# Optimization experiments

Measured on AMD Instinct MI355X. Metric: run time of the kernel, lower is better.

The kernel has to match this reference:

```python
import jax, jax.numpy as jnp
import numpy as np

N_Q = 4       # n_qubits
PATCH = 3
PAD = 1       # patch_size // 2


def _u3(theta, phi, lam):
    # U3 gate matrix (2x2 complex)
    c = jnp.cos(theta / 2)
    s = jnp.sin(theta / 2)
    row0 = jnp.stack([c + 0j, -jnp.exp(1j * lam) * s])
    row1 = jnp.stack([jnp.exp(1j * phi) * s, jnp.exp(1j * (phi + lam)) * c])
    return jnp.stack([row0, row1]).astype(jnp.complex64)


def _apply_1q(state, U, wire):
    # state: (N,2,2,2,2) complex; U: (2,2) shared or (N,2,2) batched
    s = jnp.moveaxis(state, 1 + wire, -1)
    shp = s.shape
    s = s.reshape(s.shape[0], -1, 2)
    if U.ndim == 2:
        out = jnp.einsum('ij,nrj->nri', U, s)
    else:
        out = jnp.einsum('nij,nrj->nri', U, s)
    return jnp.moveaxis(out.reshape(shp), -1, 1 + wire)


def _apply_2q(state, U4, cw, tw):
    # U4: (4,4) on (control, target) subspace ordered |c t>
    s = jnp.moveaxis(state, (1 + cw, 1 + tw), (-2, -1))
    shp = s.shape
    s = s.reshape(s.shape[0], -1, 4)
    out = jnp.einsum('ij,nrj->nri', U4, s)
    return jnp.moveaxis(out.reshape(shp), (-2, -1), (1 + cw, 1 + tw))


def setup_inputs() -> dict:
    key = jax.random.key(0)
    ks = jax.random.split(key, 8)
    B, C, H, W = 16, 64, 64, 64
    out_ch = 128
    d_in = C * PATCH * PATCH  # 576
    x = jax.random.normal(ks[0], (B, C, H, W), dtype=jnp.float32)
    fc1_w = jax.random.normal(ks[1], (N_Q, d_in), dtype=jnp.float32) * (1.0 / np.sqrt(d_in))
    fc1_b = jax.random.normal(ks[2], (N_Q,), dtype=jnp.float32) * 0.01
    u3_params = jax.random.normal(ks[3], (N_Q, 3), dtype=jnp.float32)
    cu3_params = jax.random.normal(ks[4], (N_Q, 3), dtype=jnp.float32)
    fc_w = jax.random.normal(ks[5], (out_ch, N_Q), dtype=jnp.float32) * 0.5
    fc_b = jax.random.normal(ks[6], (out_ch,), dtype=jnp.float32) * 0.01
    return {"x": x, "fc1_w": fc1_w, "fc1_b": fc1_b, "u3_params": u3_params,
            "cu3_params": cu3_params, "fc_w": fc_w, "fc_b": fc_b}


def reference(x, fc1_w, fc1_b, u3_params, cu3_params, fc_w, fc_b):
    B, C, H, W = x.shape
    xp = jnp.pad(x, ((0, 0), (0, 0), (PAD, PAD), (PAD, PAD)))
    Hout, Wout = H, W  # stride 1, same padding
    # im2col: feature order (C, di, dj) matches torch patch.reshape(B,-1)
    cols = jnp.stack([xp[:, :, di:di + Hout, dj:dj + Wout]
                      for di in range(PATCH) for dj in range(PATCH)], axis=2)  # (B,C,9,H,W)
    patches = cols.transpose(0, 3, 4, 1, 2).reshape(B, Hout * Wout, C * PATCH * PATCH)
    ang = patches @ fc1_w.T + fc1_b  # (B, P, 4) rotation angles
    Np = B * Hout * Wout
    ang = ang.reshape(Np, N_Q)
    # initial state |0000> for every (batch, patch)
    state = jnp.zeros((Np, 2 ** N_Q), jnp.complex64).at[:, 0].set(1.0)
    state = state.reshape((Np,) + (2,) * N_Q)
    # RY encoding (per-element angles)
    for w in range(N_Q):
        th = ang[:, w] / 2
        c, s = jnp.cos(th), jnp.sin(th)
        Ury = jnp.stack([jnp.stack([c, -s], -1), jnp.stack([s, c], -1)], -2).astype(jnp.complex64)
        state = _apply_1q(state, Ury, w)
    # trainable U3 on every wire
    for w in range(N_Q):
        state = _apply_1q(state, _u3(u3_params[w, 0], u3_params[w, 1], u3_params[w, 2]), w)
    # circular CU3 ring (0,1),(1,2),(2,3),(3,0)
    for w in range(N_Q):
        U = _u3(cu3_params[w, 0], cu3_params[w, 1], cu3_params[w, 2])
        U4 = jnp.eye(4, dtype=jnp.complex64).at[2:, 2:].set(U)
        state = _apply_2q(state, U4, w, (w + 1) % N_Q)
    # <Z> on each wire
    probs = state.real ** 2 + state.imag ** 2  # (Np,2,2,2,2)
    zv = jnp.array([1.0, -1.0], jnp.float32)
    expz = jnp.stack(
        [(probs * zv.reshape((1,) + (1,) * w + (2,) + (1,) * (N_Q - 1 - w))).sum(axis=(1, 2, 3, 4))
         for w in range(N_Q)], axis=1)  # (Np,4)
    out = expz.reshape(B, Hout * Wout, N_Q) @ fc_w.T + fc_b  # (B,P,out_ch)
    out_ch = fc_w.shape[0]
    # faithful to original: view(B, out_ch, side_h, side_w) on contiguous (P,out_ch)
    return out.reshape(B, out_ch, Hout, Wout)
```

## Files before the change

kernel.cpp:

```cpp
#include <hip/hip_runtime.h>
#include <hip/hip_bf16.h>
#include <math.h>

typedef unsigned short u16;
typedef unsigned int   u32;
typedef unsigned long long u64;

__device__ inline float bfbits2f(u32 lo16) {
    u32 u = lo16 << 16;
    return __builtin_bit_cast(float, u);
}
__device__ inline float bchi(u32 w) {
    return __builtin_bit_cast(float, w & 0xffff0000u);
}
__device__ inline float bclo(u32 w) {
    return __builtin_bit_cast(float, w << 16);
}
__device__ inline u16 f2bf(float f) {
    u32 u = __builtin_bit_cast(u32, f);
    u = u + 0x7fffu + ((u >> 16) & 1u);
    return (u16)(u >> 16);
}
__device__ inline float ld_param(const void* p, int i, int isbf16) {
    return isbf16 ? bfbits2f(((const u16*)p)[i]) : ((const float*)p)[i];
}

__device__ inline int sniff_bf16(const void* x, int t) {
    u32 xv = ((const u32*)x)[t & 63];
    u32 e  = (xv >> 7) & 0xFFu;
    u64 m  = __ballot(e >= 110u && e <= 130u);
    return (__popcll(m) >= 32) ? 1 : 0;
}

__global__ __launch_bounds__(256) void kA_conv(
        const void* __restrict__ x, const void* __restrict__ fc1_w,
        void* __restrict__ out) {
    __shared__ u32 tile[24 * 34];
    __shared__ float4 red4[256];
    const int t = threadIdx.x;
    const int bid = blockIdx.x;
    const int cg  = bid & 7;
    const int row = (bid >> 3) & 63;
    const int b   = bid >> 9;
    const int rowblk = bid >> 3;
    const int c0 = cg * 8;
    const int tc = t >> 6;

    const int bf = sniff_bf16(x, t);

    const int cs = __builtin_amdgcn_readfirstlane(c0 + tc * 2);
    u32 w36[36];
    if (bf) {
        const u32* fw = (const u32*)fc1_w;
#pragma unroll
        for (int k = 0; k < 36; ++k) {
            int c = cs + (k >= 18 ? 1 : 0);
            int rem = k % 18; int r = rem / 6; int p = rem % 6;
            int i0 = 2 * p, i1 = i0 + 1;
            int q0 = i0 / 3, d0 = i0 - 3 * q0;
            int q1 = i1 / 3, d1 = i1 - 3 * q1;
            int a0 = q0 * 576 + c * 9 + r * 3 + d0;
            int a1 = q1 * 576 + c * 9 + r * 3 + d1;
            u32 lo = (fw[a0 >> 1] >> (16 * (a0 & 1))) & 0xffffu;
            u32 hi = (fw[a1 >> 1] >> (16 * (a1 & 1))) & 0xffffu;
            w36[k] = lo | (hi << 16);
        }
    } else {
        const float* ff = (const float*)fc1_w;
#pragma unroll
        for (int k = 0; k < 36; ++k) {
            int c = cs + (k >= 18 ? 1 : 0);
            int rem = k % 18; int r = rem / 6; int p = rem % 6;
            int i0 = 2 * p, i1 = i0 + 1;
            int q0 = i0 / 3, d0 = i0 - 3 * q0;
            int q1 = i1 / 3, d1 = i1 - 3 * q1;
            u32 lo = f2bf(ff[q0 * 576 + c * 9 + r * 3 + d0]);
            u32 hi = f2bf(ff[q1 * 576 + c * 9 + r * 3 + d1]);
            w36[k] = lo | (hi << 16);
        }
    }

    const u32*    xu = (const u32*)x;
    const float2* xf = (const float2*)x;
    const int xbase = b * 131072;

    {
        const int jj = t & 31;
        const int g8 = t >> 5;
#pragma unroll
        for (int i = 0; i < 3; ++i) {
            int rowcl = g8 + i * 8;
            int r = rowcl >> 3, cl = rowcl & 7;
            int gr = row - 1 + r;
            u32 pk = 0;
            if (gr >= 0 && gr < 64) {
                int idx = xbase + (c0 + cl) * 2048 + gr * 32 + jj;
                if (bf) pk = xu[idx];
                else { float2 v = xf[idx];
                       pk = (u32)f2bf(v.x) | ((u32)f2bf(v.y) << 16); }
            }
            tile[rowcl * 34 + 1 + jj] = pk;
        }
        if (t < 48) { int rc = t >> 1; tile[rc * 34 + ((t & 1) ? 33 : 0)] = 0u; }
    }
    __syncthreads();

    const int j = t & 63;
    const int pj = (j + 1) >> 1;
    const int sh = (1 - (j & 1)) * 16;
    float ang0 = 0.f, ang1 = 0.f, ang2 = 0.f, ang3 = 0.f;
#pragma unroll
    for (int cc = 0; cc < 2; ++cc) {
        const int cl = tc * 2 + cc;
#pragma unroll
        for (int r = 0; r < 3; ++r) {
            const u32* rp = tile + (r * 8 + cl) * 34 + pj;
            u32 lo = rp[0], hi = rp[1];
            u64 v = (((u64)hi << 32) | lo) >> sh;
            u32 vlo = (u32)v, vhi = (u32)(v >> 32);
            float e0 = bclo(vlo);
            float e1 = bchi(vlo);
            float e2 = bclo(vhi);
            const int wb = cc * 18 + r * 6;
            u32 u0 = w36[wb], u1 = w36[wb + 1], u2 = w36[wb + 2];
            u32 u3 = w36[wb + 3], u4 = w36[wb + 4], u5 = w36[wb + 5];
            ang0 += e0 * bclo(u0) + e1 * bchi(u0) + e2 * bclo(u1);
            ang1 += e0 * bchi(u1) + e1 * bclo(u2) + e2 * bchi(u2);
            ang2 += e0 * bclo(u3) + e1 * bchi(u3) + e2 * bclo(u4);
            ang3 += e0 * bchi(u4) + e1 * bclo(u5) + e2 * bchi(u5);
        }
    }

    red4[tc * 64 + j] = make_float4(ang0, ang1, ang2, ang3);
    __syncthreads();
    if (t < 64) {
        float4 a0 = red4[t], a1 = red4[64 + t], a2 = red4[128 + t], a3 = red4[192 + t];
        float4 s = make_float4(a0.x + a1.x + a2.x + a3.x,
                               a0.y + a1.y + a2.y + a3.y,
                               a0.z + a1.z + a2.z + a3.z,
                               a0.w + a1.w + a2.w + a3.w);
        float4* part = (float4*)out;
        const int C = bf ? 1024 : 2048;
        part[rowblk * C + cg * 64 + t] = s;
    }
}

__global__ __launch_bounds__(256) void kB_circuit_fc(
        const void* __restrict__ x,
        const void* __restrict__ fc1_b, const void* __restrict__ u3p,
        const void* __restrict__ cu3p,  const void* __restrict__ fc_w,
        const void* __restrict__ fc_b,  void* __restrict__ out) {
    __shared__ float smG[64];
    __shared__ float4 smEz[64];
    const int t = threadIdx.x;
    const int bf = sniff_bf16(x, t);
    const int C = bf ? 1024 : 2048;
    const int base = blockIdx.x * C;

    float angf[4] = {0.f, 0.f, 0.f, 0.f};
    if (t < 64) {
        const float4* part = (const float4*)out;
        float ax = 0.f, ay = 0.f, az = 0.f, aw = 0.f;
#pragma unroll
        for (int g = 0; g < 8; ++g) {
            float4 a = part[base + g * 64 + t];
            ax += a.x; ay += a.y; az += a.z; aw += a.w;
        }
        angf[0] = ld_param(fc1_b, 0, bf) + ax;
        angf[1] = ld_param(fc1_b, 1, bf) + ay;
        angf[2] = ld_param(fc1_b, 2, bf) + az;
        angf[3] = ld_param(fc1_b, 3, bf) + aw;
    }
    if (t < 8) {
        int w = t & 3;
        const void* p = (t < 4) ? u3p : cu3p;
        float th = ld_param(p, w * 3 + 0, bf);
        float ph = ld_param(p, w * 3 + 1, bf);
        float la = ld_param(p, w * 3 + 2, bf);
        float c = cosf(0.5f * th), s = sinf(0.5f * th);
        float cl = cosf(la), sl = sinf(la);
        float cp = cosf(ph), sp = sinf(ph);
        float cpl = cp * cl - sp * sl, spl = sp * cl + cp * sl;
        float* m = smG + t * 8;
        m[0] = c;        m[1] = 0.f;
        m[2] = -cl * s;  m[3] = -sl * s;
        m[4] = cp * s;   m[5] = sp * s;
        m[6] = cpl * c;  m[7] = spl * c;
    }
    __syncthreads();

    if (t < 64) {
        const float* G = smG;
        float vr[4][2], vi[4][2];
#pragma unroll
        for (int w = 0; w < 4; ++w) {
            float sa, ca;
            __sincosf(0.5f * angf[w], &sa, &ca);
            const float* m = G + w * 8;
            vr[w][0] = m[0] * ca + m[2] * sa;  vi[w][0] = m[1] * ca + m[3] * sa;
            vr[w][1] = m[4] * ca + m[6] * sa;  vi[w][1] = m[5] * ca + m[7] * sa;
        }
        float t01r[4], t01i[4], t23r[4], t23i[4];
#pragma unroll
        for (int a = 0; a < 2; ++a)
#pragma unroll
            for (int bq = 0; bq < 2; ++bq) {
                t01r[a * 2 + bq] = vr[0][a] * vr[1][bq] - vi[0][a] * vi[1][bq];
                t01i[a * 2 + bq] = vr[0][a] * vi[1][bq] + vi[0][a] * vr[1][bq];
                t23r[a * 2 + bq] = vr[2][a] * vr[3][bq] - vi[2][a] * vi[3][bq];
                t23i[a * 2 + bq] = vr[2][a] * vi[3][bq] + vi[2][a] * vr[3][bq];
            }
        float ar[16], ai[16];
#pragma unroll
        for (int n = 0; n < 16; ++n) {
            int hi = n >> 2, lo = n & 3;
            ar[n] = t01r[hi] * t23r[lo] - t01i[hi] * t23i[lo];
            ai[n] = t01r[hi] * t23i[lo] + t01i[hi] * t23r[lo];
        }
#pragma unroll
        for (int w = 0; w < 4; ++w) {
            const float* m = G + 32 + w * 8;
            const int cb = 8 >> w;
            const int tb = 8 >> ((w + 1) & 3);
#pragma unroll
            for (int n = 0; n < 16; ++n) {
                if ((n & cb) != 0 && (n & tb) == 0) {
                    int n1 = n | tb;
                    float a0r = ar[n], a0i = ai[n], a1r = ar[n1], a1i = ai[n1];
                    ar[n]  = m[0] * a0r - m[1] * a0i + m[2] * a1r - m[3] * a1i;
                    ai[n]  = m[0] * a0i + m[1] * a0r + m[2] * a1i + m[3] * a1r;
                    ar[n1] = m[4] * a0r - m[5] * a0i + m[6] * a1r - m[7] * a1i;
                    ai[n1] = m[4] * a0i + m[5] * a0r + m[6] * a1i + m[7] * a1r;
                }
            }
        }
        float ez[4] = {0.f, 0.f, 0.f, 0.f};
#pragma unroll
        for (int n = 0; n < 16; ++n) {
            float pr = ar[n] * ar[n] + ai[n] * ai[n];
#pragma unroll
            for (int w = 0; w < 4; ++w)
                ez[w] += ((n >> (3 - w)) & 1) ? -pr : pr;
        }
        smEz[t] = make_float4(ez[0], ez[1], ez[2], ez[3]);
    }
    __syncthreads();

    const int og = (t & 15) * 8;
    float4 w0, w1, w2, w3, w4, w5, w6, w7, bA, bB;
    if (bf) {
        const uint4* fw4 = (const uint4*)fc_w + (og >> 1);
        uint4 qa = fw4[0], qb = fw4[1], qc = fw4[2], qd = fw4[3];
        w0 = make_float4(bclo(qa.x), bchi(qa.x), bclo(qa.y), bchi(qa.y));
        w1 = make_float4(bclo(qa.z), bchi(qa.z), bclo(qa.w), bchi(qa.w));
        w2 = make_float4(bclo(qb.x), bchi(qb.x), bclo(qb.y), bchi(qb.y));
        w3 = make_float4(bclo(qb.z), bchi(qb.z), bclo(qb.w), bchi(qb.w));
        w4 = make_float4(bclo(qc.x), bchi(qc.x), bclo(qc.y), bchi(qc.y));
        w5 = make_float4(bclo(qc.z), bchi(qc.z), bclo(qc.w), bchi(qc.w));
        w6 = make_float4(bclo(qd.x), bchi(qd.x), bclo(qd.y), bchi(qd.y));
        w7 = make_float4(bclo(qd.z), bchi(qd.z), bclo(qd.w), bchi(qd.w));
        uint4 qbb = ((const uint4*)fc_b)[og >> 3];
        bA = make_float4(bclo(qbb.x), bchi(qbb.x), bclo(qbb.y), bchi(qbb.y));
        bB = make_float4(bclo(qbb.z), bchi(qbb.z), bclo(qbb.w), bchi(qbb.w));
    } else {
        const float4* fw4 = (const float4*)fc_w + og;
        w0 = fw4[0]; w1 = fw4[1]; w2 = fw4[2]; w3 = fw4[3];
        w4 = fw4[4]; w5 = fw4[5]; w6 = fw4[6]; w7 = fw4[7];
        bA = ((const float4*)fc_b)[(og >> 2)];
        bB = ((const float4*)fc_b)[(og >> 2) + 1];
    }
#pragma unroll
    for (int ch = 0; ch < 4; ++ch) {
        const int pl = (t >> 4) + ch * 16;
        const float4 ez = smEz[pl];
        float v0 = bA.x + ez.x*w0.x + ez.y*w0.y + ez.z*w0.z + ez.w*w0.w;
        float v1 = bA.y + ez.x*w1.x + ez.y*w1.y + ez.z*w1.z + ez.w*w1.w;
        float v2 = bA.z + ez.x*w2.x + ez.y*w2.y + ez.z*w2.z + ez.w*w2.w;
        float v3 = bA.w + ez.x*w3.x + ez.y*w3.y + ez.z*w3.z + ez.w*w3.w;
        float v4 = bB.x + ez.x*w4.x + ez.y*w4.y + ez.z*w4.z + ez.w*w4.w;
        float v5 = bB.y + ez.x*w5.x + ez.y*w5.y + ez.z*w5.z + ez.w*w5.w;
        float v6 = bB.z + ez.x*w6.x + ez.y*w6.y + ez.z*w6.z + ez.w*w6.w;
        float v7 = bB.w + ez.x*w7.x + ez.y*w7.y + ez.z*w7.z + ez.w*w7.w;
        if (bf) {
            u32 p0 = (u32)f2bf(v0) | ((u32)f2bf(v1) << 16);
            u32 p1 = (u32)f2bf(v2) | ((u32)f2bf(v3) << 16);
            u32 p2 = (u32)f2bf(v4) | ((u32)f2bf(v5) << 16);
            u32 p3 = (u32)f2bf(v6) | ((u32)f2bf(v7) << 16);
            ((uint4*)out)[base + ch * 256 + t] = make_uint4(p0, p1, p2, p3);
        } else {
            float4* o = (float4*)out + (base + ch * 512 + 2 * t);
            o[0] = make_float4(v0, v1, v2, v3);
            o[1] = make_float4(v4, v5, v6, v7);
        }
    }
}

extern "C" void kernel_launch(void* const* d_in, const int* in_sizes, int n_in,
                              void* d_out, int out_size, void* d_ws, size_t ws_size,
                              hipStream_t stream) {
    (void)d_ws; (void)ws_size; (void)in_sizes; (void)n_in; (void)out_size;
    kA_conv<<<dim3(8192), dim3(256), 0, stream>>>(d_in[0], d_in[1], d_out);
    kB_circuit_fc<<<dim3(1024), dim3(256), 0, stream>>>(
        d_in[0], d_in[2], d_in[3], d_in[4], d_in[5], d_in[6], d_out);
}
```

Measured before the change: 133.7 us.

## Stage fc1 weights via LDS, move partials to workspace, widen circuit kernel blocks

```diff
diff --git a/kernel.cpp b/kernel.cpp
--- a/kernel.cpp
+++ b/kernel.cpp
@@ -5,6 +5,8 @@
 typedef unsigned short u16;
 typedef unsigned int   u32;
 typedef unsigned long long u64;
+
+#define WS_PART  4096
 
 __device__ inline float bfbits2f(u32 lo16) {
     u32 u = lo16 << 16;
@@ -34,7 +36,8 @@
 
 __global__ __launch_bounds__(256) void kA_conv(
         const void* __restrict__ x, const void* __restrict__ fc1_w,
-        void* __restrict__ out) {
+        float4* __restrict__ part) {
+    __shared__ u32 wlds[1152];
     __shared__ u32 tile[24 * 34];
     __shared__ float4 red4[256];
     const int t = threadIdx.x;
@@ -42,41 +45,38 @@
     const int cg  = bid & 7;
     const int row = (bid >> 3) & 63;
     const int b   = bid >> 9;
-    const int rowblk = bid >> 3;
     const int c0 = cg * 8;
     const int tc = t >> 6;
 
     const int bf = sniff_bf16(x, t);
 
-    const int cs = __builtin_amdgcn_readfirstlane(c0 + tc * 2);
-    u32 w36[36];
     if (bf) {
-        const u32* fw = (const u32*)fc1_w;
-#pragma unroll
-        for (int k = 0; k < 36; ++k) {
-            int c = cs + (k >= 18 ? 1 : 0);
-            int rem = k % 18; int r = rem / 6; int p = rem % 6;
-            int i0 = 2 * p, i1 = i0 + 1;
+        const u16* fw = (const u16*)fc1_w;
+        for (int idx = t; idx < 1152; idx += 256) {
+            int c = idx / 18;
+            int rem = idx - c * 18;
+            int r = rem / 6;
+            int p = rem - r * 6;
+            int i0 = 2 * p, i1 = 2 * p + 1;
             int q0 = i0 / 3, d0 = i0 - 3 * q0;
             int q1 = i1 / 3, d1 = i1 - 3 * q1;
-            int a0 = q0 * 576 + c * 9 + r * 3 + d0;
-            int a1 = q1 * 576 + c * 9 + r * 3 + d1;
-            u32 lo = (fw[a0 >> 1] >> (16 * (a0 & 1))) & 0xffffu;
-            u32 hi = (fw[a1 >> 1] >> (16 * (a1 & 1))) & 0xffffu;
-            w36[k] = lo | (hi << 16);
+            u32 lo = fw[q0 * 576 + c * 9 + r * 3 + d0];
+            u32 hi = fw[q1 * 576 + c * 9 + r * 3 + d1];
+            wlds[idx] = lo | (hi << 16);
         }
     } else {
-        const float* ff = (const float*)fc1_w;
-#pragma unroll
-        for (int k = 0; k < 36; ++k) {
-            int c = cs + (k >= 18 ? 1 : 0);
-            int rem = k % 18; int r = rem / 6; int p = rem % 6;
-            int i0 = 2 * p, i1 = i0 + 1;
+        const float* fw = (const float*)fc1_w;
+        for (int idx = t; idx < 1152; idx += 256) {
+            int c = idx / 18;
+            int rem = idx - c * 18;
+            int r = rem / 6;
+            int p = rem - r * 6;
+            int i0 = 2 * p, i1 = 2 * p + 1;
             int q0 = i0 / 3, d0 = i0 - 3 * q0;
             int q1 = i1 / 3, d1 = i1 - 3 * q1;
-            u32 lo = f2bf(ff[q0 * 576 + c * 9 + r * 3 + d0]);
-            u32 hi = f2bf(ff[q1 * 576 + c * 9 + r * 3 + d1]);
-            w36[k] = lo | (hi << 16);
+            u32 lo = f2bf(fw[q0 * 576 + c * 9 + r * 3 + d0]);
+            u32 hi = f2bf(fw[q1 * 576 + c * 9 + r * 3 + d1]);
+            wlds[idx] = lo | (hi << 16);
         }
     }
 
@@ -104,6 +104,13 @@
         if (t < 48) { int rc = t >> 1; tile[rc * 34 + ((t & 1) ? 33 : 0)] = 0u; }
     }
     __syncthreads();
+
+    const int cs = __builtin_amdgcn_readfirstlane(c0 + tc * 2);
+    const u32* wp = wlds + cs * 18;
+    u32 w36[36];
+#pragma unroll
+    for (int i = 0; i < 36; ++i)
+        w36[i] = __builtin_amdgcn_readfirstlane(wp[i]);
 
     const int j = t & 63;
     const int pj = (j + 1) >> 1;
@@ -139,9 +146,7 @@
                                a0.y + a1.y + a2.y + a3.y,
                                a0.z + a1.z + a2.z + a3.z,
                                a0.w + a1.w + a2.w + a3.w);
-        float4* part = (float4*)out;
-        const int C = bf ? 1024 : 2048;
-        part[rowblk * C + cg * 64 + t] = s;
+        part[cg * 65536 + b * 4096 + row * 64 + t] = s;
     }
 }
 
@@ -149,27 +154,19 @@
         const void* __restrict__ x,
         const void* __restrict__ fc1_b, const void* __restrict__ u3p,
         const void* __restrict__ cu3p,  const void* __restrict__ fc_w,
-        const void* __restrict__ fc_b,  void* __restrict__ out) {
+        const void* __restrict__ fc_b,  const float4* __restrict__ part,
+        void* __restrict__ out) {
     __shared__ float smG[64];
-    __shared__ float4 smEz[64];
+    __shared__ float4 smEz[256];
     const int t = threadIdx.x;
+    const int bp = blockIdx.x * 256 + t;
     const int bf = sniff_bf16(x, t);
-    const int C = bf ? 1024 : 2048;
-    const int base = blockIdx.x * C;
-
-    float angf[4] = {0.f, 0.f, 0.f, 0.f};
-    if (t < 64) {
-        const float4* part = (const float4*)out;
-        float ax = 0.f, ay = 0.f, az = 0.f, aw = 0.f;
-#pragma unroll
-        for (int g = 0; g < 8; ++g) {
-            float4 a = part[base + g * 64 + t];
-            ax += a.x; ay += a.y; az += a.z; aw += a.w;
-        }
-        angf[0] = ld_param(fc1_b, 0, bf) + ax;
-        angf[1] = ld_param(fc1_b, 1, bf) + ay;
-        angf[2] = ld_param(fc1_b, 2, bf) + az;
-        angf[3] = ld_param(fc1_b, 3, bf) + aw;
+
+    float ax = 0.f, ay = 0.f, az = 0.f, aw = 0.f;
+#pragma unroll
+    for (int g = 0; g < 8; ++g) {
+        float4 a = part[g * 65536 + bp];
+        ax += a.x; ay += a.y; az += a.z; aw += a.w;
     }
     if (t < 8) {
         int w = t & 3;
@@ -189,7 +186,13 @@
     }
     __syncthreads();
 
-    if (t < 64) {
+    float angf[4];
+    angf[0] = ld_param(fc1_b, 0, bf) + ax;
+    angf[1] = ld_param(fc1_b, 1, bf) + ay;
+    angf[2] = ld_param(fc1_b, 2, bf) + az;
+    angf[3] = ld_param(fc1_b, 3, bf) + aw;
+
+    {
         const float* G = smG;
         float vr[4][2], vi[4][2];
 #pragma unroll
@@ -270,7 +273,7 @@
         bB = ((const float4*)fc_b)[(og >> 2) + 1];
     }
 #pragma unroll
-    for (int ch = 0; ch < 4; ++ch) {
+    for (int ch = 0; ch < 16; ++ch) {
         const int pl = (t >> 4) + ch * 16;
         const float4 ez = smEz[pl];
         float v0 = bA.x + ez.x*w0.x + ez.y*w0.y + ez.z*w0.z + ez.w*w0.w;
@@ -286,9 +289,10 @@
             u32 p1 = (u32)f2bf(v2) | ((u32)f2bf(v3) << 16);
             u32 p2 = (u32)f2bf(v4) | ((u32)f2bf(v5) << 16);
             u32 p3 = (u32)f2bf(v6) | ((u32)f2bf(v7) << 16);
-            ((uint4*)out)[base + ch * 256 + t] = make_uint4(p0, p1, p2, p3);
+            ((uint4*)out)[blockIdx.x * 4096 + ch * 256 + t] =
+                make_uint4(p0, p1, p2, p3);
         } else {
-            float4* o = (float4*)out + (base + ch * 512 + 2 * t);
+            float4* o = (float4*)out + (blockIdx.x * 8192 + ch * 512 + 2 * t);
             o[0] = make_float4(v0, v1, v2, v3);
             o[1] = make_float4(v4, v5, v6, v7);
         }
@@ -298,8 +302,10 @@
 extern "C" void kernel_launch(void* const* d_in, const int* in_sizes, int n_in,
                               void* d_out, int out_size, void* d_ws, size_t ws_size,
                               hipStream_t stream) {
-    (void)d_ws; (void)ws_size; (void)in_sizes; (void)n_in; (void)out_size;
-    kA_conv<<<dim3(8192), dim3(256), 0, stream>>>(d_in[0], d_in[1], d_out);
-    kB_circuit_fc<<<dim3(1024), dim3(256), 0, stream>>>(
-        d_in[0], d_in[2], d_in[3], d_in[4], d_in[5], d_in[6], d_out);
-}
+    (void)in_sizes; (void)n_in; (void)out_size; (void)ws_size;
+    float* ws = (float*)d_ws;
+    float4* part = (float4*)(ws + WS_PART);
+    kA_conv<<<dim3(8192), dim3(256), 0, stream>>>(d_in[0], d_in[1], part);
+    kB_circuit_fc<<<dim3(256), dim3(256), 0, stream>>>(
+        d_in[0], d_in[2], d_in[3], d_in[4], d_in[5], d_in[6], part, d_out);
+}
```

Result: faster. 113.3 us (-15.3%).
